# Optimization experiments

Measured on AMD Instinct MI355X. Metric: run time of the kernel, lower is better.

Reference implementation:

```python
import jax, jax.numpy as jnp
import numpy as np

NUM_CLASSES = 32
N = 8 * 1024 * 1024  # e.g. batch of 8 segmentation masks at 1024x1024


def setup_inputs() -> dict:
    key = jax.random.key(0)
    k1, k2 = jax.random.split(key)
    y_true = jax.random.randint(k1, (N,), 0, NUM_CLASSES, dtype=jnp.int64 if jax.config.jax_enable_x64 else jnp.int32).astype(jnp.int32)
    y_pred = jax.random.randint(k2, (N,), 0, NUM_CLASSES, dtype=jnp.int32)
    return {"y_true": y_true, "y_pred": y_pred}


def reference(y_true, y_pred):
    # Equivalent to: mask = y_true != 0; cm = one_hot(y_true[mask]).T @ one_hot(y_pred[mask])
    # computed in O(N) via scatter-add on the combined (true, pred) index.
    C = NUM_CLASSES
    yt = y_true.reshape(-1)
    yp = y_pred.reshape(-1)
    w = (yt != 0).astype(jnp.float32)          # masked-out pixels contribute 0
    idx = yt * C + yp                           # combined bin index in [0, C*C)
    cm = jnp.zeros((C * C,), dtype=jnp.float32).at[idx].add(w)
    return cm.reshape(C, C)
```

## Files before the change

### kernel.cpp

```cpp
#include <hip/hip_runtime.h>

#define NUM_CLASSES 32
#define NBINS (NUM_CLASSES * NUM_CLASSES)
#define BLOCK 256
#define GRID 1024

__global__ __launch_bounds__(BLOCK) void confmat_kernel(
    const int* __restrict__ y_true,
    const int* __restrict__ y_pred,
    float* __restrict__ out,
    int n)
{
    __shared__ unsigned int hist[NBINS];
    #pragma unroll
    for (int i = threadIdx.x; i < NBINS; i += BLOCK) hist[i] = 0u;
    __syncthreads();

    const int tid    = blockIdx.x * BLOCK + threadIdx.x;
    const int stride = GRID * BLOCK;

    const int n4 = n >> 2;
    const int4* __restrict__ t4 = (const int4*)y_true;
    const int4* __restrict__ p4 = (const int4*)y_pred;
    for (int i = tid; i < n4; i += stride) {
        int4 a = t4[i];
        int4 b = p4[i];
        if (a.x != 0) atomicAdd(&hist[a.x * NUM_CLASSES + b.x], 1u);
        if (a.y != 0) atomicAdd(&hist[a.y * NUM_CLASSES + b.y], 1u);
        if (a.z != 0) atomicAdd(&hist[a.z * NUM_CLASSES + b.z], 1u);
        if (a.w != 0) atomicAdd(&hist[a.w * NUM_CLASSES + b.w], 1u);
    }

    for (int i = (n4 << 2) + tid; i < n; i += stride) {
        int a = y_true[i];
        int b = y_pred[i];
        if (a != 0) atomicAdd(&hist[a * NUM_CLASSES + b], 1u);
    }

    __syncthreads();

    #pragma unroll
    for (int i = threadIdx.x; i < NBINS; i += BLOCK) {
        unsigned int c = hist[i];
        if (c) atomicAdd(&out[i], (float)c);
    }
}

extern "C" void kernel_launch(void* const* d_in, const int* in_sizes, int n_in,
                              void* d_out, int out_size, void* d_ws, size_t ws_size,
                              hipStream_t stream) {
    const int* y_true = (const int*)d_in[0];
    const int* y_pred = (const int*)d_in[1];
    float* out = (float*)d_out;
    int n = in_sizes[0];

    hipMemsetAsync(out, 0, (size_t)out_size * sizeof(float), stream);

    confmat_kernel<<<GRID, BLOCK, 0, stream>>>(y_true, y_pred, out, n);
}
```

Baseline: 114.7 us.

## Replace global float atomics with per-block partial histograms and a reduction kernel

Each block now writes its shared-memory histogram to a workspace slice instead of issuing float atomics to the output. A second kernel sums the partial histograms in groups and issues far fewer global atomics. The grid is doubled and the main loop is unrolled four ways so more loads are in flight. The cost is an extra kernel launch and 8 MB of workspace traffic, and correctness depends on the workspace being large enough.

```diff
diff --git a/kernel.cpp b/kernel.cpp
--- a/kernel.cpp
+++ b/kernel.cpp
@@ -3,12 +3,13 @@
 #define NUM_CLASSES 32
 #define NBINS (NUM_CLASSES * NUM_CLASSES)
 #define BLOCK 256
-#define GRID 1024
+#define GRID1 2048
+#define GRID2 64
 
-__global__ __launch_bounds__(BLOCK) void confmat_kernel(
+__global__ __launch_bounds__(BLOCK) void confmat_partial(
     const int* __restrict__ y_true,
     const int* __restrict__ y_pred,
-    float* __restrict__ out,
+    unsigned int* __restrict__ ws,
     int n)
 {
     __shared__ unsigned int hist[NBINS];
@@ -17,33 +18,70 @@
     __syncthreads();
 
     const int tid    = blockIdx.x * BLOCK + threadIdx.x;
-    const int stride = GRID * BLOCK;
-
+    const int stride = GRID1 * BLOCK;
     const int n4 = n >> 2;
     const int4* __restrict__ t4 = (const int4*)y_true;
     const int4* __restrict__ p4 = (const int4*)y_pred;
-    for (int i = tid; i < n4; i += stride) {
-        int4 a = t4[i];
-        int4 b = p4[i];
-        if (a.x != 0) atomicAdd(&hist[a.x * NUM_CLASSES + b.x], 1u);
-        if (a.y != 0) atomicAdd(&hist[a.y * NUM_CLASSES + b.y], 1u);
-        if (a.z != 0) atomicAdd(&hist[a.z * NUM_CLASSES + b.z], 1u);
-        if (a.w != 0) atomicAdd(&hist[a.w * NUM_CLASSES + b.w], 1u);
+
+    int i = tid;
+    for (; i + 3 * stride < n4; i += 4 * stride) {
+        int4 a0 = t4[i];              int4 b0 = p4[i];
+        int4 a1 = t4[i + stride];     int4 b1 = p4[i + stride];
+        int4 a2 = t4[i + 2 * stride]; int4 b2 = p4[i + 2 * stride];
+        int4 a3 = t4[i + 3 * stride]; int4 b3 = p4[i + 3 * stride];
+        if (a0.x) atomicAdd(&hist[a0.x * NUM_CLASSES + b0.x], 1u);
+        if (a0.y) atomicAdd(&hist[a0.y * NUM_CLASSES + b0.y], 1u);
+        if (a0.z) atomicAdd(&hist[a0.z * NUM_CLASSES + b0.z], 1u);
+        if (a0.w) atomicAdd(&hist[a0.w * NUM_CLASSES + b0.w], 1u);
+        if (a1.x) atomicAdd(&hist[a1.x * NUM_CLASSES + b1.x], 1u);
+        if (a1.y) atomicAdd(&hist[a1.y * NUM_CLASSES + b1.y], 1u);
+        if (a1.z) atomicAdd(&hist[a1.z * NUM_CLASSES + b1.z], 1u);
+        if (a1.w) atomicAdd(&hist[a1.w * NUM_CLASSES + b1.w], 1u);
+        if (a2.x) atomicAdd(&hist[a2.x * NUM_CLASSES + b2.x], 1u);
+        if (a2.y) atomicAdd(&hist[a2.y * NUM_CLASSES + b2.y], 1u);
+        if (a2.z) atomicAdd(&hist[a2.z * NUM_CLASSES + b2.z], 1u);
+        if (a2.w) atomicAdd(&hist[a2.w * NUM_CLASSES + b2.w], 1u);
+        if (a3.x) atomicAdd(&hist[a3.x * NUM_CLASSES + b3.x], 1u);
+        if (a3.y) atomicAdd(&hist[a3.y * NUM_CLASSES + b3.y], 1u);
+        if (a3.z) atomicAdd(&hist[a3.z * NUM_CLASSES + b3.z], 1u);
+        if (a3.w) atomicAdd(&hist[a3.w * NUM_CLASSES + b3.w], 1u);
     }
-
-    for (int i = (n4 << 2) + tid; i < n; i += stride) {
-        int a = y_true[i];
-        int b = y_pred[i];
-        if (a != 0) atomicAdd(&hist[a * NUM_CLASSES + b], 1u);
+    for (; i < n4; i += stride) {
+        int4 a = t4[i]; int4 b = p4[i];
+        if (a.x) atomicAdd(&hist[a.x * NUM_CLASSES + b.x], 1u);
+        if (a.y) atomicAdd(&hist[a.y * NUM_CLASSES + b.y], 1u);
+        if (a.z) atomicAdd(&hist[a.z * NUM_CLASSES + b.z], 1u);
+        if (a.w) atomicAdd(&hist[a.w * NUM_CLASSES + b.w], 1u);
+    }
+    for (int j = (n4 << 2) + tid; j < n; j += stride) {
+        int a = y_true[j]; int b = y_pred[j];
+        if (a) atomicAdd(&hist[a * NUM_CLASSES + b], 1u);
     }
 
     __syncthreads();
 
-    #pragma unroll
-    for (int i = threadIdx.x; i < NBINS; i += BLOCK) {
-        unsigned int c = hist[i];
-        if (c) atomicAdd(&out[i], (float)c);
+    uint4* __restrict__ w4 = (uint4*)(ws + (size_t)blockIdx.x * NBINS);
+    const uint4* __restrict__ h4 = (const uint4*)hist;
+    w4[threadIdx.x] = h4[threadIdx.x];
+}
+
+__global__ __launch_bounds__(BLOCK) void confmat_reduce(
+    const unsigned int* __restrict__ ws,
+    float* __restrict__ out)
+{
+    const int t = threadIdx.x;
+    const int pbase = blockIdx.x * (GRID1 / GRID2);
+    const uint4* __restrict__ w4 = (const uint4*)ws;
+    unsigned int sx = 0, sy = 0, sz = 0, sw = 0;
+    #pragma unroll 8
+    for (int p = 0; p < GRID1 / GRID2; ++p) {
+        uint4 v = w4[(size_t)(pbase + p) * (NBINS / 4) + t];
+        sx += v.x; sy += v.y; sz += v.z; sw += v.w;
     }
+    atomicAdd(&out[4 * t + 0], (float)sx);
+    atomicAdd(&out[4 * t + 1], (float)sy);
+    atomicAdd(&out[4 * t + 2], (float)sz);
+    atomicAdd(&out[4 * t + 3], (float)sw);
 }
 
 extern "C" void kernel_launch(void* const* d_in, const int* in_sizes, int n_in,
@@ -52,9 +90,11 @@
     const int* y_true = (const int*)d_in[0];
     const int* y_pred = (const int*)d_in[1];
     float* out = (float*)d_out;
+    unsigned int* ws = (unsigned int*)d_ws;
     int n = in_sizes[0];
 
     hipMemsetAsync(out, 0, (size_t)out_size * sizeof(float), stream);
 
-    confmat_kernel<<<GRID, BLOCK, 0, stream>>>(y_true, y_pred, out, n);
+    confmat_partial<<<GRID1, BLOCK, 0, stream>>>(y_true, y_pred, ws, n);
+    confmat_reduce<<<GRID2, BLOCK, 0, stream>>>(ws, out);
 }
```

After: 102.0 us. -11.0%, faster.
